# Performance work log

Hardware: AMD Instinct MI355X
Metric: run time of the kernel (lower is better)

Reference implementation:

```python
import jax, jax.numpy as jnp
import numpy as np

N, D, F1, F2, F3, H = 4096, 512, 64, 32, 16, 4
ALPHA = 0.2  # LeakyReLU negative slope
NEG = -9e15


def setup_inputs() -> dict:
    key = jax.random.key(0)
    ks = jax.random.split(key, 11)
    # sparse binary adjacency with self loops (adj.to_dense() in original)
    adj = (jax.random.uniform(ks[1], (N, N)) < 0.01).astype(jnp.float32)
    adj = jnp.maximum(adj, jnp.eye(N, dtype=jnp.float32))
    return {
        "x": jax.random.normal(ks[0], (N, D), jnp.float32),
        "adj": adj,
        "W_heads": jax.random.normal(ks[2], (H, D, F1), jnp.float32) * 0.05,
        "a_heads": jax.random.normal(ks[3], (H, 2 * F1, 1), jnp.float32) * 0.05,
        "W_att": jax.random.normal(ks[4], (H * F1, F1), jnp.float32) * 0.05,
        "a_att": jax.random.normal(ks[5], (2 * F1, 1), jnp.float32) * 0.05,
        "W1": jax.random.normal(ks[6], (F1, F2), jnp.float32) * 0.05,
        "W2": jax.random.normal(ks[7], (F2, F3), jnp.float32) * 0.05,
        "W3": jax.random.normal(ks[8], (F2, F3), jnp.float32) * 0.05,
        "eps": jax.random.normal(ks[9], (N, F3), jnp.float32),
    }


def _gat(x, adj, W, a, out_dim):
    Wh = x @ W                                   # [N, F]
    e = (Wh @ a[:out_dim]) + (Wh @ a[out_dim:]).T  # [N,1] + [1,N] -> [N,N]
    e = jax.nn.leaky_relu(e, negative_slope=ALPHA)
    att = jax.nn.softmax(jnp.where(adj > 0, e, NEG), axis=-1)
    return jax.nn.elu(att @ Wh)                  # [N, F]


def reference(x, adj, W_heads, a_heads, W_att, a_att, W1, W2, W3, eps):
    # multi-head GAT, concat along feature dim
    heads = jax.vmap(lambda W, a: _gat(x, adj, W, a, F1))(W_heads, a_heads)  # [H,N,F1]
    cat = jnp.transpose(heads, (1, 0, 2)).reshape(N, H * F1)
    gc_att = _gat(cat, adj, W_att, a_att, F1)    # [N, F1]
    # GCN layers (dropout off, no bias): spmm(adj, x @ W)
    h1 = jax.nn.relu(adj @ (gc_att @ W1))        # [N, F2]
    mu = adj @ (h1 @ W2)                         # [N, F3]
    logvar = adj @ (h1 @ W3)                     # [N, F3]
    # reparameterize (vae_bool=True): eps * exp(logvar) + mu
    z = eps * jnp.exp(logvar) + mu
    adj_rec = z @ z.T                            # inner-product decoder [N,N]
    return adj_rec, mu, logvar
```

## Files before the change

### kernel.cpp

```cpp
#include <hip/hip_runtime.h>
#include <math.h>

#define NN 4096
#define DD 512
#define F1 64
#define F2 32
#define F3 16
#define NH 4
#define ALPHA 0.2f
#define CAP 160

__device__ __forceinline__ float lrelu(float e) { return (e >= 0.f) ? e : ALPHA * e; }

__global__ void k_csr(const float* __restrict__ adj, int* __restrict__ colidx,
                      int* __restrict__ deg) {
  __shared__ int cnt;
  int i = blockIdx.x, tid = threadIdx.x;
  if (tid == 0) cnt = 0;
  __syncthreads();
  const float4* arow = (const float4*)(adj + (size_t)i * NN);
  for (int t = tid; t < NN / 4; t += 256) {
    float4 v = arow[t];
    int base = t * 4;
    if (v.x != 0.f) { int p = atomicAdd(&cnt, 1); if (p < CAP) colidx[(size_t)i * CAP + p] = base; }
    if (v.y != 0.f) { int p = atomicAdd(&cnt, 1); if (p < CAP) colidx[(size_t)i * CAP + p] = base + 1; }
    if (v.z != 0.f) { int p = atomicAdd(&cnt, 1); if (p < CAP) colidx[(size_t)i * CAP + p] = base + 2; }
    if (v.w != 0.f) { int p = atomicAdd(&cnt, 1); if (p < CAP) colidx[(size_t)i * CAP + p] = base + 3; }
  }
  __syncthreads();
  if (tid == 0) deg[i] = cnt < CAP ? cnt : CAP;
}

__device__ __forceinline__ void wh_load(const float* __restrict__ Wf,
                                        const float xsrow[8][DD], int rg, int g,
                                        float* w, float4* xv) {
#pragma unroll
  for (int h = 0; h < 4; ++h)
#pragma unroll
    for (int kk = 0; kk < 8; ++kk)
      w[h * 8 + kk] = Wf[(size_t)h * DD * F1 + (size_t)(g + kk) * F1];
#pragma unroll
  for (int r = 0; r < 4; ++r) {
    xv[r * 2 + 0] = *(const float4*)&xsrow[rg * 4 + r][g];
    xv[r * 2 + 1] = *(const float4*)&xsrow[rg * 4 + r][g + 4];
  }
}

__device__ __forceinline__ void wh_fma(const float* w, const float4* xv,
                                       float acc[4][4]) {
#pragma unroll
  for (int r = 0; r < 4; ++r) {
    float4 a = xv[r * 2], b = xv[r * 2 + 1];
#pragma unroll
    for (int h = 0; h < 4; ++h) {
      const float* wp = w + h * 8;
      float s = acc[r][h];
      s = fmaf(a.x, wp[0], s); s = fmaf(a.y, wp[1], s);
      s = fmaf(a.z, wp[2], s); s = fmaf(a.w, wp[3], s);
      s = fmaf(b.x, wp[4], s); s = fmaf(b.y, wp[5], s);
      s = fmaf(b.z, wp[6], s); s = fmaf(b.w, wp[7], s);
      acc[r][h] = s;
    }
  }
}

__global__ __launch_bounds__(256) void k_wh_heads(
    const float* __restrict__ x, const float* __restrict__ W_heads,
    const float* __restrict__ a_heads, float* __restrict__ Whcat,
    float* __restrict__ s1, float* __restrict__ s2) {
  __shared__ float xs[8][DD];
  __shared__ float pbuf[2][4][4][64];
  int tid = threadIdx.x;
  int r0 = blockIdx.x * 8;
  const float4* xsrc = (const float4*)(x + (size_t)r0 * DD);
  float4* xd = (float4*)xs;
  xd[tid] = xsrc[tid];
  xd[tid + 256] = xsrc[tid + 256];
  xd[tid + 512] = xsrc[tid + 512];
  xd[tid + 768] = xsrc[tid + 768];
  __syncthreads();
  int f = tid & 63;
  int w = tid >> 6;
  int rg = w >> 1;
  int kh = w & 1;
  int k0 = kh * 256;
  const float* Wf = W_heads + f;
  float acc[4][4] = {};
  float wA[32], wB[32];
  float4 xA[8], xB[8];
  wh_load(Wf, xs, rg, k0, wA, xA);
  for (int k = k0; k < k0 + 256; k += 16) {
    if (k + 8 < k0 + 256) wh_load(Wf, xs, rg, k + 8, wB, xB);
    wh_fma(wA, xA, acc);
    if (k + 16 < k0 + 256) wh_load(Wf, xs, rg, k + 16, wA, xA);
    wh_fma(wB, xB, acc);
  }
  if (kh == 1) {
#pragma unroll
    for (int r = 0; r < 4; ++r)
#pragma unroll
      for (int h = 0; h < 4; ++h) pbuf[rg][r][h][f] = acc[r][h];
  }
  __syncthreads();
  if (kh == 0) {
#pragma unroll
    for (int r = 0; r < 4; ++r)
#pragma unroll
      for (int h = 0; h < 4; ++h) acc[r][h] += pbuf[rg][r][h][f];
    int rb = r0 + rg * 4;
#pragma unroll
    for (int r = 0; r < 4; ++r)
#pragma unroll
      for (int h = 0; h < 4; ++h)
        Whcat[(size_t)(rb + r) * (NH * F1) + h * 64 + f] = acc[r][h];
#pragma unroll
    for (int h = 0; h < 4; ++h) {
      float a1 = a_heads[h * 2 * F1 + f];
      float a2 = a_heads[h * 2 * F1 + F1 + f];
#pragma unroll
      for (int r = 0; r < 4; ++r) {
        float v1 = acc[r][h] * a1;
        float v2 = acc[r][h] * a2;
#pragma unroll
        for (int off = 32; off > 0; off >>= 1) {
          v1 += __shfl_down(v1, off, 64);
          v2 += __shfl_down(v2, off, 64);
        }
        if (f == 0) {
          s1[h * NN + rb + r] = v1;
          s2[h * NN + rb + r] = v2;
        }
      }
    }
  }
}

__global__ void k_gat_heads(const int* __restrict__ colidx, const int* __restrict__ deg,
                            const float* __restrict__ Whcat,
                            const float* __restrict__ s1, const float* __restrict__ s2,
                            float* __restrict__ cat) {
  __shared__ int idx[CAP];
  __shared__ float wsh[NH][CAP];
  int i = blockIdx.x, tid = threadIdx.x;
  int c = deg[i];
  for (int t = tid; t < c; t += 256) idx[t] = colidx[(size_t)i * CAP + t];
  __syncthreads();
  int h = tid >> 6;
  int f = tid & 63;
  const float* s2h = s2 + h * NN;
  float s1v = s1[h * NN + i];
  float M = -INFINITY;
  for (int k = f; k < c; k += 64) {
    float v = s2h[idx[k]];
    wsh[h][k] = v;
    M = fmaxf(M, v);
  }
#pragma unroll
  for (int off = 32; off > 0; off >>= 1) M = fmaxf(M, __shfl_down(M, off, 64));
  M = __shfl(M, 0, 64);
  float m = lrelu(s1v + M);
  float lsum = 0.f;
  for (int k = f; k < c; k += 64) {
    float w = __expf(lrelu(s1v + wsh[h][k]) - m);
    wsh[h][k] = w;
    lsum += w;
  }
#pragma unroll
  for (int off = 32; off > 0; off >>= 1) lsum += __shfl_down(lsum, off, 64);
  float linv = 1.f / __shfl(lsum, 0, 64);
  __syncthreads();
  const float* base = Whcat + h * 64 + f;
  float a0 = 0.f, a1 = 0.f, a2 = 0.f, a3 = 0.f;
  int k = 0;
  for (; k + 4 <= c; k += 4) {
    int j0 = idx[k], j1 = idx[k + 1], j2 = idx[k + 2], j3 = idx[k + 3];
    a0 = fmaf(wsh[h][k],     base[(size_t)j0 * 256], a0);
    a1 = fmaf(wsh[h][k + 1], base[(size_t)j1 * 256], a1);
    a2 = fmaf(wsh[h][k + 2], base[(size_t)j2 * 256], a2);
    a3 = fmaf(wsh[h][k + 3], base[(size_t)j3 * 256], a3);
  }
  for (; k < c; ++k) a0 = fmaf(wsh[h][k], base[(size_t)idx[k] * 256], a0);
  float o = (a0 + a1 + a2 + a3) * linv;
  cat[(size_t)i * (NH * F1) + tid] = (o > 0.f) ? o : expm1f(o);
}

__global__ void k_wh2(const float* __restrict__ cat,
                      const float* __restrict__ W_att,
                      const float* __restrict__ a_att,
                      float* __restrict__ Wh2,
                      float* __restrict__ s1b, float* __restrict__ s2b) {
  const int ROWS = 8;
  __shared__ float cs[ROWS][NH * F1];
  int tid = threadIdx.x;
  int r0 = blockIdx.x * ROWS;
  const float4* csrc = (const float4*)(cat + (size_t)r0 * 256);
  for (int t = tid; t < ROWS * 256 / 4; t += 256) ((float4*)cs)[t] = csrc[t];
  __syncthreads();
  int g = tid >> 6;
  int f = tid & 63;
  float a1 = a_att[f], a2 = a_att[64 + f];
  const float* W = W_att + f;
#pragma unroll
  for (int rr = 0; rr < 2; ++rr) {
    int r = g * 2 + rr;
    float acc = 0.f;
    for (int k = 0; k < 256; k += 4) {
      float4 cv = *(const float4*)&cs[r][k];
      acc = fmaf(cv.x, W[(k + 0) * 64], acc);
      acc = fmaf(cv.y, W[(k + 1) * 64], acc);
      acc = fmaf(cv.z, W[(k + 2) * 64], acc);
      acc = fmaf(cv.w, W[(k + 3) * 64], acc);
    }
    Wh2[(size_t)(r0 + r) * 64 + f] = acc;
    float v1 = acc * a1, v2 = acc * a2;
#pragma unroll
    for (int off = 32; off > 0; off >>= 1) {
      v1 += __shfl_down(v1, off, 64);
      v2 += __shfl_down(v2, off, 64);
    }
    if (f == 0) { s1b[r0 + r] = v1; s2b[r0 + r] = v2; }
  }
}

__global__ void k_gat2t1(const int* __restrict__ colidx, const int* __restrict__ deg,
                         const float* __restrict__ Wh2,
                         const float* __restrict__ s1b, const float* __restrict__ s2b,
                         const float* __restrict__ W1, float* __restrict__ t1) {
  __shared__ int idx4[4][CAP];
  __shared__ float wsh4[4][CAP];
  __shared__ float grow[4][64];
  __shared__ float W1s[F1 * F2];
  int tid = threadIdx.x;
  int w = tid >> 6, f = tid & 63;
  int i = blockIdx.x * 4 + w;
  int c = deg[i];
  for (int t = tid; t < F1 * F2; t += 256) W1s[t] = W1[t];
  for (int k = f; k < c; k += 64) idx4[w][k] = colidx[(size_t)i * CAP + k];
  __syncthreads();
  float s1v = s1b[i];
  float M = -INFINITY;
  for (int k = f; k < c; k += 64) {
    float v = s2b[idx4[w][k]];
    wsh4[w][k] = v;
    M = fmaxf(M, v);
  }
#pragma unroll
  for (int off = 32; off > 0; off >>= 1) M = fmaxf(M, __shfl_down(M, off, 64));
  M = __shfl(M, 0, 64);
  float m = lrelu(s1v + M);
  float lsum = 0.f;
  for (int k = f; k < c; k += 64) {
    float wv = __expf(lrelu(s1v + wsh4[w][k]) - m);
    wsh4[w][k] = wv;
    lsum += wv;
  }
#pragma unroll
  for (int off = 32; off > 0; off >>= 1) lsum += __shfl_down(lsum, off, 64);
  float linv = 1.f / __shfl(lsum, 0, 64);
  __syncthreads();
  const float* base = Wh2 + f;
  float a0 = 0.f, a1 = 0.f, a2 = 0.f, a3 = 0.f;
  int k = 0;
  for (; k + 4 <= c; k += 4) {
    int j0 = idx4[w][k], j1 = idx4[w][k + 1], j2 = idx4[w][k + 2], j3 = idx4[w][k + 3];
    a0 = fmaf(wsh4[w][k],     base[(size_t)j0 * 64], a0);
    a1 = fmaf(wsh4[w][k + 1], base[(size_t)j1 * 64], a1);
    a2 = fmaf(wsh4[w][k + 2], base[(size_t)j2 * 64], a2);
    a3 = fmaf(wsh4[w][k + 3], base[(size_t)j3 * 64], a3);
  }
  for (; k < c; ++k) a0 = fmaf(wsh4[w][k], base[(size_t)idx4[w][k] * 64], a0);
  float o = (a0 + a1 + a2 + a3) * linv;
  grow[w][f] = (o > 0.f) ? o : expm1f(o);
  __syncthreads();
  if (f < F2) {
    float acc = 0.f;
#pragma unroll 8
    for (int kk = 0; kk < F1; ++kk) acc = fmaf(grow[w][kk], W1s[kk * F2 + f], acc);
    t1[(size_t)i * F2 + f] = acc;
  }
}

__global__ void k_gcn1t23(const int* __restrict__ colidx, const int* __restrict__ deg,
                          const float* __restrict__ t1,
                          const float* __restrict__ W2, const float* __restrict__ W3,
                          float* __restrict__ t23) {
  __shared__ int idx4[4][CAP];
  __shared__ float hrow[4][F2];
  __shared__ float Wc[F2 * 32];
  int tid = threadIdx.x;
  int w = tid >> 6, lane = tid & 63;
  int nb = lane >> 5, g = lane & 31;
  int i = blockIdx.x * 4 + w;
  int c = deg[i];
  for (int t = tid; t < F2 * 32; t += 256) {
    int kk = t >> 5, gg = t & 31;
    Wc[t] = (gg < 16) ? W2[kk * 16 + gg] : W3[kk * 16 + (gg - 16)];
  }
  for (int k = lane; k < c; k += 64) idx4[w][k] = colidx[(size_t)i * CAP + k];
  __syncthreads();
  float a0 = 0.f, a1 = 0.f;
  int k = nb;
  for (; k + 2 < c; k += 4) {
    a0 += t1[(size_t)idx4[w][k] * F2 + g];
    a1 += t1[(size_t)idx4[w][k + 2] * F2 + g];
  }
  for (; k < c; k += 2) a0 += t1[(size_t)idx4[w][k] * F2 + g];
  float tot = a0 + a1;
  tot += __shfl_xor(tot, 32, 64);
  float h1v = fmaxf(tot, 0.f);
  if (nb == 0) hrow[w][g] = h1v;
  __syncthreads();
  if (lane < 32) {
    float acc = 0.f;
#pragma unroll 8
    for (int kk = 0; kk < F2; ++kk) acc = fmaf(hrow[w][kk], Wc[kk * 32 + lane], acc);
    t23[(size_t)i * 32 + lane] = acc;
  }
}

__global__ void k_gcn2(const int* __restrict__ colidx, const int* __restrict__ deg,
                       const float* __restrict__ t23, const float* __restrict__ eps,
                       float* __restrict__ mu_out, float* __restrict__ lv_out,
                       float* __restrict__ z) {
  __shared__ int idx4[4][CAP];
  int tid = threadIdx.x;
  int w = tid >> 6, lane = tid & 63;
  int nb = lane >> 5, g = lane & 31;
  int i = blockIdx.x * 4 + w;
  int c = deg[i];
  for (int k = lane; k < c; k += 64) idx4[w][k] = colidx[(size_t)i * CAP + k];
  __syncthreads();
  float a0 = 0.f, a1 = 0.f;
  int k = nb;
  for (; k + 2 < c; k += 4) {
    a0 += t23[(size_t)idx4[w][k] * 32 + g];
    a1 += t23[(size_t)idx4[w][k + 2] * 32 + g];
  }
  for (; k < c; k += 2) a0 += t23[(size_t)idx4[w][k] * 32 + g];
  float tot = a0 + a1;
  tot += __shfl_xor(tot, 32, 64);
  float lvv = __shfl(tot, (lane & 31) + 16, 64);
  if (lane < 16) {
    mu_out[(size_t)i * 16 + g] = tot;
    z[(size_t)i * 16 + g] = eps[(size_t)i * 16 + g] * expf(lvv) + tot;
  } else if (lane < 32) {
    lv_out[(size_t)i * 16 + (g - 16)] = tot;
  }
}

__global__ void k_zzt(const float* __restrict__ z, float* __restrict__ out) {
  __shared__ float zr[64][17];
  __shared__ float zc[64][17];
  int bj = blockIdx.x, bi = blockIdx.y;
  int tid = threadIdx.x;
  for (int t = tid; t < 64 * 16; t += 256) {
    int r = t >> 4, kk = t & 15;
    zr[r][kk] = z[(size_t)(bi * 64 + r) * 16 + kk];
    zc[r][kk] = z[(size_t)(bj * 64 + r) * 16 + kk];
  }
  __syncthreads();
  int rg = tid >> 4;
  int cg = tid & 15;
  float acc[4][4] = {};
  for (int kk = 0; kk < 16; ++kk) {
    float av[4], bv[4];
#pragma unroll
    for (int t = 0; t < 4; ++t) av[t] = zr[rg * 4 + t][kk];
#pragma unroll
    for (int t = 0; t < 4; ++t) bv[t] = zc[cg * 4 + t][kk];
#pragma unroll
    for (int r = 0; r < 4; ++r)
#pragma unroll
      for (int cc = 0; cc < 4; ++cc) acc[r][cc] = fmaf(av[r], bv[cc], acc[r][cc]);
  }
#pragma unroll
  for (int r = 0; r < 4; ++r) {
    float4 v = make_float4(acc[r][0], acc[r][1], acc[r][2], acc[r][3]);
    *(float4*)&out[(size_t)(bi * 64 + rg * 4 + r) * NN + bj * 64 + cg * 4] = v;
  }
}

extern "C" void kernel_launch(void* const* d_in, const int* in_sizes, int n_in,
                              void* d_out, int out_size, void* d_ws, size_t ws_size,
                              hipStream_t stream) {
  const float* x       = (const float*)d_in[0];
  const float* adj     = (const float*)d_in[1];
  const float* W_heads = (const float*)d_in[2];
  const float* a_heads = (const float*)d_in[3];
  const float* W_att   = (const float*)d_in[4];
  const float* a_att   = (const float*)d_in[5];
  const float* W1      = (const float*)d_in[6];
  const float* W2      = (const float*)d_in[7];
  const float* W3      = (const float*)d_in[8];
  const float* eps     = (const float*)d_in[9];

  float* out = (float*)d_out;
  float* adj_rec = out;
  float* mu_out  = out + (size_t)NN * NN;
  float* lv_out  = mu_out + (size_t)NN * F3;

  float* ws = (float*)d_ws;
  float* Whcat = ws;               ws += (size_t)NN * NH * F1;
  float* s1    = ws;               ws += (size_t)NH * NN;
  float* s2    = ws;               ws += (size_t)NH * NN;
  float* cat   = ws;               ws += (size_t)NN * NH * F1;
  float* Wh2   = ws;               ws += (size_t)NN * F1;
  float* s1b   = ws;               ws += NN;
  float* s2b   = ws;               ws += NN;
  float* t1    = ws;               ws += (size_t)NN * F2;
  float* t23   = ws;               ws += (size_t)NN * 2 * F3;
  float* z     = ws;               ws += (size_t)NN * F3;
  int*   colidx = (int*)ws;        ws += (size_t)NN * CAP;
  int*   deg    = (int*)ws;        ws += NN;

  k_csr<<<NN, 256, 0, stream>>>(adj, colidx, deg);
  k_wh_heads<<<NN / 8, 256, 0, stream>>>(x, W_heads, a_heads, Whcat, s1, s2);
  k_gat_heads<<<NN, 256, 0, stream>>>(colidx, deg, Whcat, s1, s2, cat);
  k_wh2<<<NN / 8, 256, 0, stream>>>(cat, W_att, a_att, Wh2, s1b, s2b);
  k_gat2t1<<<NN / 4, 256, 0, stream>>>(colidx, deg, Wh2, s1b, s2b, W1, t1);
  k_gcn1t23<<<NN / 4, 256, 0, stream>>>(colidx, deg, t1, W2, W3, t23);
  k_gcn2<<<NN / 4, 256, 0, stream>>>(colidx, deg, t23, eps, mu_out, lv_out, z);
  k_zzt<<<dim3(64, 64), 256, 0, stream>>>(z, adj_rec);
}
```

Measured before the change: 230.4 us.

## Replace per-row head projection with tiled double-buffered shared-memory GEMM

```diff
diff --git a/kernel.cpp b/kernel.cpp
--- a/kernel.cpp
+++ b/kernel.cpp
@@ -31,106 +31,98 @@
   if (tid == 0) deg[i] = cnt < CAP ? cnt : CAP;
 }
 
-__device__ __forceinline__ void wh_load(const float* __restrict__ Wf,
-                                        const float xsrow[8][DD], int rg, int g,
-                                        float* w, float4* xv) {
-#pragma unroll
-  for (int h = 0; h < 4; ++h)
-#pragma unroll
-    for (int kk = 0; kk < 8; ++kk)
-      w[h * 8 + kk] = Wf[(size_t)h * DD * F1 + (size_t)(g + kk) * F1];
-#pragma unroll
-  for (int r = 0; r < 4; ++r) {
-    xv[r * 2 + 0] = *(const float4*)&xsrow[rg * 4 + r][g];
-    xv[r * 2 + 1] = *(const float4*)&xsrow[rg * 4 + r][g + 4];
-  }
-}
-
-__device__ __forceinline__ void wh_fma(const float* w, const float4* xv,
-                                       float acc[4][4]) {
-#pragma unroll
-  for (int r = 0; r < 4; ++r) {
-    float4 a = xv[r * 2], b = xv[r * 2 + 1];
-#pragma unroll
-    for (int h = 0; h < 4; ++h) {
-      const float* wp = w + h * 8;
-      float s = acc[r][h];
-      s = fmaf(a.x, wp[0], s); s = fmaf(a.y, wp[1], s);
-      s = fmaf(a.z, wp[2], s); s = fmaf(a.w, wp[3], s);
-      s = fmaf(b.x, wp[4], s); s = fmaf(b.y, wp[5], s);
-      s = fmaf(b.z, wp[6], s); s = fmaf(b.w, wp[7], s);
-      acc[r][h] = s;
-    }
-  }
-}
-
-__global__ __launch_bounds__(256) void k_wh_heads(
+__global__ __launch_bounds__(256) void k_wh_gemm(
     const float* __restrict__ x, const float* __restrict__ W_heads,
     const float* __restrict__ a_heads, float* __restrict__ Whcat,
     float* __restrict__ s1, float* __restrict__ s2) {
-  __shared__ float xs[8][DD];
-  __shared__ float pbuf[2][4][4][64];
-  int tid = threadIdx.x;
-  int r0 = blockIdx.x * 8;
-  const float4* xsrc = (const float4*)(x + (size_t)r0 * DD);
-  float4* xd = (float4*)xs;
-  xd[tid] = xsrc[tid];
-  xd[tid + 256] = xsrc[tid + 256];
-  xd[tid + 512] = xsrc[tid + 512];
-  xd[tid + 768] = xsrc[tid + 768];
-  __syncthreads();
-  int f = tid & 63;
-  int w = tid >> 6;
-  int rg = w >> 1;
-  int kh = w & 1;
-  int k0 = kh * 256;
-  const float* Wf = W_heads + f;
+  __shared__ float As[2][32][65];
+  __shared__ float Bs[2][32][64];
+  int tid = threadIdx.x;
+  int h = blockIdx.y;
+  int r0 = blockIdx.x * 64;
+  const float* Wh = W_heads + (size_t)h * DD * F1;
+
+  int sr = tid >> 3, sq = tid & 7;
+  int bk = tid >> 4, bf = tid & 15;
+  int rg = tid >> 4, cg = tid & 15;
+
+  const float* xa0 = x + (size_t)(r0 + sr) * DD;
+  const float* xa1 = x + (size_t)(r0 + sr + 32) * DD;
+
+  float4 pa0 = *(const float4*)(xa0 + sq * 4);
+  float4 pa1 = *(const float4*)(xa1 + sq * 4);
+  float4 pb0 = *(const float4*)(Wh + (size_t)bk * F1 + bf * 4);
+  float4 pb1 = *(const float4*)(Wh + (size_t)(bk + 16) * F1 + bf * 4);
+  {
+    float* a0p = &As[0][sq * 4][sr];
+    a0p[0] = pa0.x; a0p[65] = pa0.y; a0p[130] = pa0.z; a0p[195] = pa0.w;
+    float* a1p = &As[0][sq * 4][sr + 32];
+    a1p[0] = pa1.x; a1p[65] = pa1.y; a1p[130] = pa1.z; a1p[195] = pa1.w;
+    *(float4*)&Bs[0][bk][bf * 4] = pb0;
+    *(float4*)&Bs[0][bk + 16][bf * 4] = pb1;
+  }
+  __syncthreads();
+
   float acc[4][4] = {};
-  float wA[32], wB[32];
-  float4 xA[8], xB[8];
-  wh_load(Wf, xs, rg, k0, wA, xA);
-  for (int k = k0; k < k0 + 256; k += 16) {
-    if (k + 8 < k0 + 256) wh_load(Wf, xs, rg, k + 8, wB, xB);
-    wh_fma(wA, xA, acc);
-    if (k + 16 < k0 + 256) wh_load(Wf, xs, rg, k + 16, wA, xA);
-    wh_fma(wB, xB, acc);
-  }
-  if (kh == 1) {
-#pragma unroll
-    for (int r = 0; r < 4; ++r)
-#pragma unroll
-      for (int h = 0; h < 4; ++h) pbuf[rg][r][h][f] = acc[r][h];
-  }
-  __syncthreads();
-  if (kh == 0) {
-#pragma unroll
-    for (int r = 0; r < 4; ++r)
-#pragma unroll
-      for (int h = 0; h < 4; ++h) acc[r][h] += pbuf[rg][r][h][f];
-    int rb = r0 + rg * 4;
-#pragma unroll
-    for (int r = 0; r < 4; ++r)
-#pragma unroll
-      for (int h = 0; h < 4; ++h)
-        Whcat[(size_t)(rb + r) * (NH * F1) + h * 64 + f] = acc[r][h];
-#pragma unroll
-    for (int h = 0; h < 4; ++h) {
-      float a1 = a_heads[h * 2 * F1 + f];
-      float a2 = a_heads[h * 2 * F1 + F1 + f];
-#pragma unroll
-      for (int r = 0; r < 4; ++r) {
-        float v1 = acc[r][h] * a1;
-        float v2 = acc[r][h] * a2;
-#pragma unroll
-        for (int off = 32; off > 0; off >>= 1) {
-          v1 += __shfl_down(v1, off, 64);
-          v2 += __shfl_down(v2, off, 64);
-        }
-        if (f == 0) {
-          s1[h * NN + rb + r] = v1;
-          s2[h * NN + rb + r] = v2;
-        }
-      }
+  for (int c = 0; c < 16; ++c) {
+    int cb = c & 1;
+    if (c < 15) {
+      int k0 = (c + 1) * 32;
+      pa0 = *(const float4*)(xa0 + k0 + sq * 4);
+      pa1 = *(const float4*)(xa1 + k0 + sq * 4);
+      pb0 = *(const float4*)(Wh + (size_t)(k0 + bk) * F1 + bf * 4);
+      pb1 = *(const float4*)(Wh + (size_t)(k0 + bk + 16) * F1 + bf * 4);
+    }
+#pragma unroll
+    for (int kk = 0; kk < 32; ++kk) {
+      float4 av = *(const float4*)&As[cb][kk][rg * 4];
+      float4 bv = *(const float4*)&Bs[cb][kk][cg * 4];
+      acc[0][0] = fmaf(av.x, bv.x, acc[0][0]);
+      acc[0][1] = fmaf(av.x, bv.y, acc[0][1]);
+      acc[0][2] = fmaf(av.x, bv.z, acc[0][2]);
+      acc[0][3] = fmaf(av.x, bv.w, acc[0][3]);
+      acc[1][0] = fmaf(av.y, bv.x, acc[1][0]);
+      acc[1][1] = fmaf(av.y, bv.y, acc[1][1]);
+      acc[1][2] = fmaf(av.y, bv.z, acc[1][2]);
+      acc[1][3] = fmaf(av.y, bv.w, acc[1][3]);
+      acc[2][0] = fmaf(av.z, bv.x, acc[2][0]);
+      acc[2][1] = fmaf(av.z, bv.y, acc[2][1]);
+      acc[2][2] = fmaf(av.z, bv.z, acc[2][2]);
+      acc[2][3] = fmaf(av.z, bv.w, acc[2][3]);
+      acc[3][0] = fmaf(av.w, bv.x, acc[3][0]);
+      acc[3][1] = fmaf(av.w, bv.y, acc[3][1]);
+      acc[3][2] = fmaf(av.w, bv.z, acc[3][2]);
+      acc[3][3] = fmaf(av.w, bv.w, acc[3][3]);
+    }
+    if (c < 15) {
+      int nb = cb ^ 1;
+      float* a0p = &As[nb][sq * 4][sr];
+      a0p[0] = pa0.x; a0p[65] = pa0.y; a0p[130] = pa0.z; a0p[195] = pa0.w;
+      float* a1p = &As[nb][sq * 4][sr + 32];
+      a1p[0] = pa1.x; a1p[65] = pa1.y; a1p[130] = pa1.z; a1p[195] = pa1.w;
+      *(float4*)&Bs[nb][bk][bf * 4] = pb0;
+      *(float4*)&Bs[nb][bk + 16][bf * 4] = pb1;
+      __syncthreads();
+    }
+  }
+
+  float4 a1v = *(const float4*)&a_heads[h * 2 * F1 + cg * 4];
+  float4 a2v = *(const float4*)&a_heads[h * 2 * F1 + F1 + cg * 4];
+#pragma unroll
+  for (int r = 0; r < 4; ++r) {
+    int row = r0 + rg * 4 + r;
+    *(float4*)&Whcat[(size_t)row * (NH * F1) + h * 64 + cg * 4] =
+        make_float4(acc[r][0], acc[r][1], acc[r][2], acc[r][3]);
+    float v1 = acc[r][0] * a1v.x + acc[r][1] * a1v.y + acc[r][2] * a1v.z + acc[r][3] * a1v.w;
+    float v2 = acc[r][0] * a2v.x + acc[r][1] * a2v.y + acc[r][2] * a2v.z + acc[r][3] * a2v.w;
+#pragma unroll
+    for (int off = 8; off > 0; off >>= 1) {
+      v1 += __shfl_down(v1, off, 16);
+      v2 += __shfl_down(v2, off, 16);
+    }
+    if (cg == 0) {
+      s1[h * NN + row] = v1;
+      s2[h * NN + row] = v2;
     }
   }
 }
@@ -414,7 +406,7 @@
   int*   deg    = (int*)ws;        ws += NN;
 
   k_csr<<<NN, 256, 0, stream>>>(adj, colidx, deg);
-  k_wh_heads<<<NN / 8, 256, 0, stream>>>(x, W_heads, a_heads, Whcat, s1, s2);
+  k_wh_gemm<<<dim3(64, 4), 256, 0, stream>>>(x, W_heads, a_heads, Whcat, s1, s2);
   k_gat_heads<<<NN, 256, 0, stream>>>(colidx, deg, Whcat, s1, s2, cat);
   k_wh2<<<NN / 8, 256, 0, stream>>>(cat, W_att, a_att, Wh2, s1b, s2b);
   k_gat2t1<<<NN / 4, 256, 0, stream>>>(colidx, deg, Wh2, s1b, s2b, W1, t1);
```

Result: faster. 224.6 us (-2.5%).
